# Kernel tuning notes

Measured on AMD Instinct MI355X. Metric: run time of the kernel, lower is better.

The kernel has to match this reference:

```python
import jax, jax.numpy as jnp
import numpy as np

N, CIN, COUT, E, NDIR = 65536, 128, 128, 589824, 9


def sel_conv(x, src, dst, sel, W, b):
    # x: [N, Cin]; W: [D, Cin, Cout]; edges j->i: out[i] += x[j] @ W[sel]
    n = x.shape[0]
    xs = x[src]  # [E, Cin] gather
    out = jnp.zeros((n, W.shape[2]), x.dtype)
    for d in range(W.shape[0]):  # fixed small direction count (9 or 1)
        m = (sel == d).astype(x.dtype)[:, None]
        agg = jax.ops.segment_sum(xs * m, dst, num_segments=n)  # [N, Cin]
        out = out + agg @ W[d]
    return out + b


def bn_eval(x, g, be, rm, rv, eps=1e-5):
    return (x - rm) * (g * jax.lax.rsqrt(rv + eps)) + be


def setup_inputs() -> dict:
    key = jax.random.key(0)
    ks = jax.random.split(key, 24)
    s = 0.05
    inp = {
        "x": jax.random.normal(ks[0], (N, CIN), jnp.float32),
        "edge_index": jax.random.randint(ks[1], (2, E), 0, N),
        "selections": jax.random.randint(ks[2], (E,), 0, NDIR),
        "W1": jax.random.normal(ks[3], (NDIR, CIN, COUT), jnp.float32) * s,
        "b1": jax.random.normal(ks[4], (COUT,), jnp.float32) * s,
        "g1": 1.0 + jax.random.normal(ks[5], (COUT,), jnp.float32) * s,
        "be1": jax.random.normal(ks[6], (COUT,), jnp.float32) * s,
        "rm1": jax.random.normal(ks[7], (COUT,), jnp.float32) * s,
        "rv1": 0.5 + jax.random.uniform(ks[8], (COUT,), jnp.float32),
        "W2": jax.random.normal(ks[9], (NDIR, COUT, COUT), jnp.float32) * s,
        "b2": jax.random.normal(ks[10], (COUT,), jnp.float32) * s,
        "g2": 1.0 + jax.random.normal(ks[11], (COUT,), jnp.float32) * s,
        "be2": jax.random.normal(ks[12], (COUT,), jnp.float32) * s,
        "rm2": jax.random.normal(ks[13], (COUT,), jnp.float32) * s,
        "rv2": 0.5 + jax.random.uniform(ks[14], (COUT,), jnp.float32),
        "W3": jax.random.normal(ks[15], (1, CIN, COUT), jnp.float32) * s,
        "b3": jax.random.normal(ks[16], (COUT,), jnp.float32) * s,
        "g3": 1.0 + jax.random.normal(ks[17], (COUT,), jnp.float32) * s,
        "be3": jax.random.normal(ks[18], (COUT,), jnp.float32) * s,
        "rm3": jax.random.normal(ks[19], (COUT,), jnp.float32) * s,
        "rv3": 0.5 + jax.random.uniform(ks[20], (COUT,), jnp.float32),
    }
    return inp


def reference(x, edge_index, selections, W1, b1, g1, be1, rm1, rv1,
              W2, b2, g2, be2, rm2, rv2, W3, b3, g3, be3, rm3, rv3):
    src, dst = edge_index[0], edge_index[1]
    # conv1: SelectionConv(3x3) + BN + ELU
    h = jax.nn.elu(bn_eval(sel_conv(x, src, dst, selections, W1, b1), g1, be1, rm1, rv1))
    # conv2: SelectionConv(3x3) + BN + ELU
    h = jax.nn.elu(bn_eval(sel_conv(h, src, dst, selections, W2, b2), g2, be2, rm2, rv2))
    # conv3: SelectionConv(1x1) shortcut (only selection-0 edges)
    sc = sel_conv(x, src, dst, selections, W3, b3)
    return jax.nn.elu(bn_eval(h + sc, g3, be3, rm3, rv3))
```

## Files before the change

### kernel.cpp

```cpp
#include <hip/hip_runtime.h>
#include <hip/hip_bf16.h>
#include <math.h>

#define N_NODES 65536
#define NDIR 9
#define NEDGE 589824
#define TILE_M 32
#define CAP 512
#define APITCH 136

typedef __attribute__((ext_vector_type(8))) short short8;
typedef __attribute__((ext_vector_type(4))) float f32x4;

__device__ inline float bf2f(unsigned short u){ return __uint_as_float(((unsigned int)u)<<16); }
__device__ inline unsigned short f2bf(float f){
  unsigned int x = __float_as_uint(f);
  x += 0x7fff + ((x>>16)&1);
  return (unsigned short)(x>>16);
}
__device__ inline float elu1(float x){ return x>0.f ? x : expm1f(x); }

__device__ inline void acc8(f32x4& a0, f32x4& a1, short8 v){
  a0[0] += bf2f((unsigned short)v[0]); a0[1] += bf2f((unsigned short)v[1]);
  a0[2] += bf2f((unsigned short)v[2]); a0[3] += bf2f((unsigned short)v[3]);
  a1[0] += bf2f((unsigned short)v[4]); a1[1] += bf2f((unsigned short)v[5]);
  a1[2] += bf2f((unsigned short)v[6]); a1[3] += bf2f((unsigned short)v[7]);
}

__global__ void prep_all(const float* __restrict__ x, unsigned short* __restrict__ xb,
                         const float* __restrict__ W1, const float* __restrict__ W2,
                         const float* __restrict__ W3,
                         const float* __restrict__ b1, const float* __restrict__ g1,
                         const float* __restrict__ be1, const float* __restrict__ rm1,
                         const float* __restrict__ rv1,
                         const float* __restrict__ b2, const float* __restrict__ g2,
                         const float* __restrict__ be2, const float* __restrict__ rm2,
                         const float* __restrict__ rv2,
                         const float* __restrict__ b3, const float* __restrict__ g3,
                         const float* __restrict__ be3, const float* __restrict__ rm3,
                         const float* __restrict__ rv3,
                         unsigned short* __restrict__ Wt1, unsigned short* __restrict__ Wt2,
                         float* __restrict__ bias1, float* __restrict__ bias2,
                         float* __restrict__ bias3, float* __restrict__ s3v,
                         int* __restrict__ hist){
  const float eps = 1e-5f;
  int b = blockIdx.x, tid = threadIdx.x;
  if (b < 64){
    int4 z = {0,0,0,0};
    *(int4*)&hist[(b*256 + tid)*4] = z;
  } else if (b < 1280){
    int idx = (b - 64)*256 + tid;
    if (idx < 1280*128) {
      int n = idx >> 7, k = idx & 127;
      float v;
      if (n < 1152) { int d = n >> 7, c = n & 127;
        float s = g1[c]*rsqrtf(rv1[c]+eps); v = W1[(d*128 + k)*128 + c] * s; }
      else { int c = n - 1152;
        float s = g3[c]*rsqrtf(rv3[c]+eps); v = W3[k*128 + c] * s; }
      Wt1[idx] = f2bf(v);
    } else {
      int j = idx - 1280*128;
      int n = j >> 7, k = j & 127;
      int d = n >> 7, c = n & 127;
      float s = g2[c]*rsqrtf(rv2[c]+eps);
      Wt2[j] = f2bf(W2[(d*128 + k)*128 + c] * s);
    }
  } else if (b == 1280){
    if (tid < 128){
      int c = tid;
      float s1 = g1[c]*rsqrtf(rv1[c]+eps);
      bias1[c] = (b1[c]-rm1[c])*s1 + be1[c];
      float s2 = g2[c]*rsqrtf(rv2[c]+eps);
      bias2[c] = (b2[c]-rm2[c])*s2 + be2[c];
      float s3 = g3[c]*rsqrtf(rv3[c]+eps);
      bias3[c] = (b3[c]-rm3[c])*s3 + be3[c];
      s3v[c] = s3;
    }
  } else {
    int i = ((b - 1281)*256 + tid)*8;
    f32x4 f0 = *(const f32x4*)(x + i);
    f32x4 f1 = *(const f32x4*)(x + i + 4);
    short8 t;
    #pragma unroll
    for (int j = 0; j < 4; j++){ t[j] = (short)f2bf(f0[j]); t[4+j] = (short)f2bf(f1[j]); }
    *(short8*)(xb + i) = t;
  }
}

__global__ void hist_k(const int* __restrict__ dst, int* __restrict__ hist){
  int e = blockIdx.x*256 + threadIdx.x;
  atomicAdd(&hist[dst[e]], 1);
}

__global__ void scan1_k(const int* __restrict__ in, int* __restrict__ out, int* __restrict__ bsum){
  __shared__ int wsum[4];
  int t = threadIdx.x;
  int base = blockIdx.x*1024 + t*4;
  int4 v = *(const int4*)(in + base);
  int s = v.x + v.y + v.z + v.w;
  int lane = t & 63, w = t >> 6;
  int inc = s;
  #pragma unroll
  for (int o = 1; o < 64; o <<= 1){ int n = __shfl_up(inc, o); if (lane >= o) inc += n; }
  if (lane == 63) wsum[w] = inc;
  __syncthreads();
  int acc = 0;
  for (int i = 0; i < w; i++) acc += wsum[i];
  int ex = acc + inc - s;
  out[base] = ex; out[base+1] = ex + v.x; out[base+2] = ex + v.x + v.y; out[base+3] = ex + v.x + v.y + v.z;
  if (t == 255) bsum[blockIdx.x] = acc + inc;
}

__global__ void scan3_k(int* __restrict__ rs, const int* __restrict__ bsumx, int* __restrict__ cursor){
  int i = blockIdx.x*256 + threadIdx.x;
  int v = rs[i] + bsumx[i >> 10];
  rs[i] = v; cursor[i] = v;
  if (i == 0) rs[N_NODES] = NEDGE;
}

__global__ void scatter_k(const int* __restrict__ src, const int* __restrict__ dst,
                          const int* __restrict__ sel,
                          int* __restrict__ cursor, int* __restrict__ sorted){
  int e = blockIdx.x*256 + threadIdx.x;
  int pos = atomicAdd(&cursor[dst[e]], 1);
  sorted[pos] = src[e] | (sel[e] << 16);
}

__device__ __forceinline__ void mfma_tile(f32x4 acc[2][2],
                                          const unsigned short* agg,
                                          const unsigned short* __restrict__ Wd,
                                          int w, int q, int r){
  #pragma unroll
  for (int kk = 0; kk < 4; kk++){
    const unsigned short* wp = Wd + (size_t)(w*32 + r)*128 + kk*32 + q*8;
    short8 b0 = *(const short8*)wp;
    short8 b1 = *(const short8*)(wp + 16*128);
    #pragma unroll
    for (int mt = 0; mt < 2; mt++){
      short8 av = *(const short8*)&agg[(mt*16 + r)*APITCH + kk*32 + q*8];
      acc[mt][0] = __builtin_amdgcn_mfma_f32_16x16x32_bf16(av, b0, acc[mt][0], 0, 0, 0);
      acc[mt][1] = __builtin_amdgcn_mfma_f32_16x16x32_bf16(av, b1, acc[mt][1], 0, 0, 0);
    }
  }
}

template<int IS_L2>
__global__ __launch_bounds__(256, 8) void layer_k(
    const unsigned short* __restrict__ H,
    const unsigned short* __restrict__ X,
    const unsigned short* __restrict__ Wf,
    const unsigned short* __restrict__ W3f,
    const int* __restrict__ rs, const int* __restrict__ sorted,
    const float* __restrict__ biasA, const float* __restrict__ bias3,
    const float* __restrict__ s3v,
    unsigned short* __restrict__ outB, float* __restrict__ outF){
  __shared__ __align__(16) unsigned short agg[TILE_M*APITCH];
  __shared__ int skey[CAP];
  __shared__ unsigned short skey2[CAP];
  __shared__ int rsl2[TILE_M + 1];
  __shared__ int po[TILE_M*9];
  __shared__ int wo[TILE_M*9];
  const int tid = threadIdx.x;
  const int w = tid >> 6, lane = tid & 63;
  const int q = lane >> 4, r = lane & 15;
  const int rid = tid >> 4, c = tid & 15;
  const int m0 = blockIdx.x * TILE_M;

  if (tid <= TILE_M) rsl2[tid] = rs[m0 + tid];
  for (int i = tid; i < TILE_M*9; i += 256) wo[i] = 0;
  __syncthreads();
  const int lo = rsl2[0];
  const int cnt = rsl2[TILE_M] - lo;
  for (int i = tid; i < cnt && i < CAP; i += 256) skey[i] = sorted[lo + i];
  __syncthreads();

  {
    const int nl8 = tid >> 3, sub = tid & 7;
    int s = rsl2[nl8] - lo, e = rsl2[nl8+1] - lo;
    if (e > CAP) e = CAP;
    for (int i = s + sub; i < e; i += 8)
      atomicAdd(&wo[nl8*9 + (skey[i] >> 16)], 1);
  }
  __syncthreads();
  if (tid < TILE_M){
    int base = rsl2[tid] - lo;
    if (base > CAP) base = CAP;
    #pragma unroll
    for (int d = 0; d < 9; d++){
      int b = tid*9 + d;
      po[b] = base;
      int cc = wo[b];
      wo[b] = base;
      base += cc;
    }
  }
  __syncthreads();
  {
    const int nl8 = tid >> 3, sub = tid & 7;
    int s = rsl2[nl8] - lo, e = rsl2[nl8+1] - lo;
    if (e > CAP) e = CAP;
    for (int i = s + sub; i < e; i += 8){
      int k = skey[i];
      int pos = atomicAdd(&wo[nl8*9 + (k >> 16)], 1);
      skey2[pos] = (unsigned short)k;
    }
  }
  __syncthreads();

  f32x4 acc[2][2];
  #pragma unroll
  for (int mt = 0; mt < 2; mt++){ acc[mt][0] = (f32x4){0,0,0,0}; acc[mt][1] = (f32x4){0,0,0,0}; }

  #pragma unroll 1
  for (int d = 0; d < 9; d++){
    if (d) __syncthreads();
    {
      int b = rid*9 + d;
      int s = po[b], e = wo[b];
      f32x4 a0 = {0,0,0,0}, a1 = {0,0,0,0};
      for (int i = s; i < e; i++){
        int key = skey2[i];
        short8 v = *(const short8*)(H + (size_t)key*128 + c*8);
        acc8(a0, a1, v);
      }
      int ts = rsl2[rid] - lo; if (ts < CAP) ts = CAP;
      int te = rsl2[rid+1] - lo;
      for (int i = ts; i < te; i++){
        int k = sorted[lo + i];
        if ((k >> 16) == d){
          short8 v = *(const short8*)(H + (size_t)(k & 0xFFFF)*128 + c*8);
          acc8(a0, a1, v);
        }
      }
      short8 o;
      o[0]=(short)f2bf(a0[0]); o[1]=(short)f2bf(a0[1]); o[2]=(short)f2bf(a0[2]); o[3]=(short)f2bf(a0[3]);
      o[4]=(short)f2bf(a1[0]); o[5]=(short)f2bf(a1[1]); o[6]=(short)f2bf(a1[2]); o[7]=(short)f2bf(a1[3]);
      *(short8*)&agg[rid*APITCH + c*8] = o;
    }
    {
      int b = (16 + rid)*9 + d;
      int s = po[b], e = wo[b];
      f32x4 a0 = {0,0,0,0}, a1 = {0,0,0,0};
      for (int i = s; i < e; i++){
        int key = skey2[i];
        short8 v = *(const short8*)(H + (size_t)key*128 + c*8);
        acc8(a0, a1, v);
      }
      int ts = rsl2[16+rid] - lo; if (ts < CAP) ts = CAP;
      int te = rsl2[16+rid+1] - lo;
      for (int i = ts; i < te; i++){
        int k = sorted[lo + i];
        if ((k >> 16) == d){
          short8 v = *(const short8*)(H + (size_t)(k & 0xFFFF)*128 + c*8);
          acc8(a0, a1, v);
        }
      }
      short8 o;
      o[0]=(short)f2bf(a0[0]); o[1]=(short)f2bf(a0[1]); o[2]=(short)f2bf(a0[2]); o[3]=(short)f2bf(a0[3]);
      o[4]=(short)f2bf(a1[0]); o[5]=(short)f2bf(a1[1]); o[6]=(short)f2bf(a1[2]); o[7]=(short)f2bf(a1[3]);
      *(short8*)&agg[(16 + rid)*APITCH + c*8] = o;
    }
    __syncthreads();
    mfma_tile(acc, agg, Wf + (size_t)d*128*128, w, q, r);
  }

  if constexpr (!IS_L2){
    #pragma unroll
    for (int mt = 0; mt < 2; mt++)
      #pragma unroll
      for (int n2 = 0; n2 < 2; n2++){
        int col = w*32 + n2*16 + r;
        float bA = biasA[col];
        #pragma unroll
        for (int rr = 0; rr < 4; rr++){
          int row = m0 + mt*16 + q*4 + rr;
          outB[(size_t)row*128 + col] = f2bf(elu1(acc[mt][n2][rr] + bA));
        }
      }
  } else {
    __syncthreads();
    #pragma unroll
    for (int t2 = 0; t2 < 2; t2++){
      int nl = t2*16 + rid;
      int b = nl*9;
      int s = po[b], e = wo[b];
      f32x4 a0 = {0,0,0,0}, a1 = {0,0,0,0};
      for (int i = s; i < e; i++){
        int key = skey2[i];
        short8 v = *(const short8*)(X + (size_t)key*128 + c*8);
        acc8(a0, a1, v);
      }
      int ts = rsl2[nl] - lo; if (ts < CAP) ts = CAP;
      int te = rsl2[nl+1] - lo;
      for (int i = ts; i < te; i++){
        int k = sorted[lo + i];
        if ((k >> 16) == 0){
          short8 v = *(const short8*)(X + (size_t)(k & 0xFFFF)*128 + c*8);
          acc8(a0, a1, v);
        }
      }
      short8 o;
      o[0]=(short)f2bf(a0[0]); o[1]=(short)f2bf(a0[1]); o[2]=(short)f2bf(a0[2]); o[3]=(short)f2bf(a0[3]);
      o[4]=(short)f2bf(a1[0]); o[5]=(short)f2bf(a1[1]); o[6]=(short)f2bf(a1[2]); o[7]=(short)f2bf(a1[3]);
      *(short8*)&agg[nl*APITCH + c*8] = o;
    }
    __syncthreads();
    f32x4 sca[2][2];
    #pragma unroll
    for (int mt = 0; mt < 2; mt++){ sca[mt][0] = (f32x4){0,0,0,0}; sca[mt][1] = (f32x4){0,0,0,0}; }
    mfma_tile(sca, agg, W3f, w, q, r);
    #pragma unroll
    for (int mt = 0; mt < 2; mt++)
      #pragma unroll
      for (int n2 = 0; n2 < 2; n2++){
        int col = w*32 + n2*16 + r;
        float bA = biasA[col], b3 = bias3[col], s3 = s3v[col];
        #pragma unroll
        for (int rr = 0; rr < 4; rr++){
          int row = m0 + mt*16 + q*4 + rr;
          float h = elu1(acc[mt][n2][rr] + bA);
          outF[(size_t)row*128 + col] = elu1(h*s3 + sca[mt][n2][rr] + b3);
        }
      }
  }
}

extern "C" void kernel_launch(void* const* d_in, const int* in_sizes, int n_in,
                              void* d_out, int out_size, void* d_ws, size_t ws_size,
                              hipStream_t stream){
  const float* x   = (const float*)d_in[0];
  const int*   ei  = (const int*)d_in[1];
  const int*   sel = (const int*)d_in[2];
  const float* W1  = (const float*)d_in[3];
  const float* b1  = (const float*)d_in[4];
  const float* g1  = (const float*)d_in[5];
  const float* be1 = (const float*)d_in[6];
  const float* rm1 = (const float*)d_in[7];
  const float* rv1 = (const float*)d_in[8];
  const float* W2  = (const float*)d_in[9];
  const float* b2  = (const float*)d_in[10];
  const float* g2  = (const float*)d_in[11];
  const float* be2 = (const float*)d_in[12];
  const float* rm2 = (const float*)d_in[13];
  const float* rv2 = (const float*)d_in[14];
  const float* W3  = (const float*)d_in[15];
  const float* b3  = (const float*)d_in[16];
  const float* g3  = (const float*)d_in[17];
  const float* be3 = (const float*)d_in[18];
  const float* rm3 = (const float*)d_in[19];
  const float* rv3 = (const float*)d_in[20];

  char* ws = (char*)d_ws;
  unsigned short* xb   = (unsigned short*)(ws);
  unsigned short* h1   = (unsigned short*)(ws + 16777216);
  unsigned short* Wt1  = (unsigned short*)(ws + 33554432);
  unsigned short* Wt2  = (unsigned short*)(ws + 33882112);
  float* bias1  = (float*)(ws + 34177024);
  float* bias2  = bias1 + 128;
  float* bias3  = bias1 + 256;
  float* s3v    = bias1 + 384;
  int* hist     = (int*)(ws + 34179072);
  int* rs       = (int*)(ws + 36538368);
  int* cursor   = (int*)(ws + 38897920);
  int* bsum     = (int*)(ws + 41257216);
  int* bsumx    = (int*)(ws + 41261312);
  int* bsumT    = (int*)(ws + 41265408);
  int* sorted   = (int*)(ws + 41265664);

  const int* srcp = ei;
  const int* dstp = ei + NEDGE;

  prep_all<<<5377, 256, 0, stream>>>(x, xb, W1, W2, W3,
                                     b1, g1, be1, rm1, rv1,
                                     b2, g2, be2, rm2, rv2,
                                     b3, g3, be3, rm3, rv3,
                                     Wt1, Wt2, bias1, bias2, bias3, s3v, hist);
  hist_k<<<NEDGE/256, 256, 0, stream>>>(dstp, hist);
  scan1_k<<<N_NODES/1024, 256, 0, stream>>>(hist, rs, bsum);
  scan1_k<<<1, 256, 0, stream>>>(bsum, bsumx, bsumT);
  scan3_k<<<N_NODES/256, 256, 0, stream>>>(rs, bsumx, cursor);
  scatter_k<<<NEDGE/256, 256, 0, stream>>>(srcp, dstp, sel, cursor, sorted);

  layer_k<0><<<2048, 256, 0, stream>>>(xb, nullptr, Wt1, nullptr, rs, sorted,
                                       bias1, nullptr, nullptr, h1, nullptr);
  layer_k<1><<<2048, 256, 0, stream>>>(h1, xb, Wt2, Wt1 + 1152*128, rs, sorted,
                                       bias2, bias3, s3v, nullptr, (float*)d_out);
}
```

Before: 364.0 us.

## Fuse preprocessing, histogram, scan and scatter into one cooperative kernel

Replaces six separate launches (prep, histogram, two scan passes, scan fixup, scatter) with a single cooperative kernel of 1024 blocks that uses grid-stride loops and grid.sync() between phases. This removes per-launch overhead and the gaps between small kernels. In exchange, the grid-wide barriers cost time, occupancy is limited to a co-resident grid, and the single-block scan phases leave most blocks idle.

```diff
diff --git a/kernel.cpp b/kernel.cpp
--- a/kernel.cpp
+++ b/kernel.cpp
@@ -1,6 +1,9 @@
 #include <hip/hip_runtime.h>
 #include <hip/hip_bf16.h>
+#include <hip/hip_cooperative_groups.h>
 #include <math.h>
+
+namespace cg = cooperative_groups;
 
 #define N_NODES 65536
 #define NDIR 9
@@ -27,29 +30,38 @@
   a1[2] += bf2f((unsigned short)v[6]); a1[3] += bf2f((unsigned short)v[7]);
 }
 
-__global__ void prep_all(const float* __restrict__ x, unsigned short* __restrict__ xb,
-                         const float* __restrict__ W1, const float* __restrict__ W2,
-                         const float* __restrict__ W3,
-                         const float* __restrict__ b1, const float* __restrict__ g1,
-                         const float* __restrict__ be1, const float* __restrict__ rm1,
-                         const float* __restrict__ rv1,
-                         const float* __restrict__ b2, const float* __restrict__ g2,
-                         const float* __restrict__ be2, const float* __restrict__ rm2,
-                         const float* __restrict__ rv2,
-                         const float* __restrict__ b3, const float* __restrict__ g3,
-                         const float* __restrict__ be3, const float* __restrict__ rm3,
-                         const float* __restrict__ rv3,
-                         unsigned short* __restrict__ Wt1, unsigned short* __restrict__ Wt2,
-                         float* __restrict__ bias1, float* __restrict__ bias2,
-                         float* __restrict__ bias3, float* __restrict__ s3v,
-                         int* __restrict__ hist){
+__global__ __launch_bounds__(256, 4) void chain_k(
+    const float* __restrict__ x, unsigned short* __restrict__ xb,
+    const float* __restrict__ W1, const float* __restrict__ W2,
+    const float* __restrict__ W3,
+    const float* __restrict__ b1, const float* __restrict__ g1,
+    const float* __restrict__ be1, const float* __restrict__ rm1,
+    const float* __restrict__ rv1,
+    const float* __restrict__ b2, const float* __restrict__ g2,
+    const float* __restrict__ be2, const float* __restrict__ rm2,
+    const float* __restrict__ rv2,
+    const float* __restrict__ b3, const float* __restrict__ g3,
+    const float* __restrict__ be3, const float* __restrict__ rm3,
+    const float* __restrict__ rv3,
+    unsigned short* __restrict__ Wt1, unsigned short* __restrict__ Wt2,
+    float* __restrict__ bias1, float* __restrict__ bias2,
+    float* __restrict__ bias3, float* __restrict__ s3v,
+    int* __restrict__ hist, int* __restrict__ rs, int* __restrict__ cursor,
+    int* __restrict__ bsum, int* __restrict__ bsumx,
+    const int* __restrict__ src, const int* __restrict__ dst,
+    const int* __restrict__ sel, int* __restrict__ sorted){
+  cg::grid_group grid = cg::this_grid();
+  __shared__ int wsum[4];
   const float eps = 1e-5f;
-  int b = blockIdx.x, tid = threadIdx.x;
-  if (b < 64){
+  const int b = blockIdx.x, tid = threadIdx.x;
+  const int gtid = b*256 + tid;
+  const int gstride = gridDim.x*256;
+
+  for (int i = gtid; i < N_NODES/4; i += gstride){
     int4 z = {0,0,0,0};
-    *(int4*)&hist[(b*256 + tid)*4] = z;
-  } else if (b < 1280){
-    int idx = (b - 64)*256 + tid;
+    ((int4*)hist)[i] = z;
+  }
+  for (int idx = gtid; idx < (1280*128 + 1152*128); idx += gstride){
     if (idx < 1280*128) {
       int n = idx >> 7, k = idx & 127;
       float v;
@@ -65,65 +77,69 @@
       float s = g2[c]*rsqrtf(rv2[c]+eps);
       Wt2[j] = f2bf(W2[(d*128 + k)*128 + c] * s);
     }
-  } else if (b == 1280){
-    if (tid < 128){
-      int c = tid;
-      float s1 = g1[c]*rsqrtf(rv1[c]+eps);
-      bias1[c] = (b1[c]-rm1[c])*s1 + be1[c];
-      float s2 = g2[c]*rsqrtf(rv2[c]+eps);
-      bias2[c] = (b2[c]-rm2[c])*s2 + be2[c];
-      float s3 = g3[c]*rsqrtf(rv3[c]+eps);
-      bias3[c] = (b3[c]-rm3[c])*s3 + be3[c];
-      s3v[c] = s3;
-    }
-  } else {
-    int i = ((b - 1281)*256 + tid)*8;
-    f32x4 f0 = *(const f32x4*)(x + i);
-    f32x4 f1 = *(const f32x4*)(x + i + 4);
+  }
+  if (gtid < 128){
+    int c = gtid;
+    float s1 = g1[c]*rsqrtf(rv1[c]+eps);
+    bias1[c] = (b1[c]-rm1[c])*s1 + be1[c];
+    float s2 = g2[c]*rsqrtf(rv2[c]+eps);
+    bias2[c] = (b2[c]-rm2[c])*s2 + be2[c];
+    float s3 = g3[c]*rsqrtf(rv3[c]+eps);
+    bias3[c] = (b3[c]-rm3[c])*s3 + be3[c];
+    s3v[c] = s3;
+  }
+  for (int i = gtid; i < N_NODES*128/8; i += gstride){
+    f32x4 f0 = *(const f32x4*)(x + i*8);
+    f32x4 f1 = *(const f32x4*)(x + i*8 + 4);
     short8 t;
     #pragma unroll
     for (int j = 0; j < 4; j++){ t[j] = (short)f2bf(f0[j]); t[4+j] = (short)f2bf(f1[j]); }
-    *(short8*)(xb + i) = t;
-  }
-}
-
-__global__ void hist_k(const int* __restrict__ dst, int* __restrict__ hist){
-  int e = blockIdx.x*256 + threadIdx.x;
-  atomicAdd(&hist[dst[e]], 1);
-}
-
-__global__ void scan1_k(const int* __restrict__ in, int* __restrict__ out, int* __restrict__ bsum){
-  __shared__ int wsum[4];
-  int t = threadIdx.x;
-  int base = blockIdx.x*1024 + t*4;
-  int4 v = *(const int4*)(in + base);
-  int s = v.x + v.y + v.z + v.w;
-  int lane = t & 63, w = t >> 6;
-  int inc = s;
-  #pragma unroll
-  for (int o = 1; o < 64; o <<= 1){ int n = __shfl_up(inc, o); if (lane >= o) inc += n; }
-  if (lane == 63) wsum[w] = inc;
-  __syncthreads();
-  int acc = 0;
-  for (int i = 0; i < w; i++) acc += wsum[i];
-  int ex = acc + inc - s;
-  out[base] = ex; out[base+1] = ex + v.x; out[base+2] = ex + v.x + v.y; out[base+3] = ex + v.x + v.y + v.z;
-  if (t == 255) bsum[blockIdx.x] = acc + inc;
-}
-
-__global__ void scan3_k(int* __restrict__ rs, const int* __restrict__ bsumx, int* __restrict__ cursor){
-  int i = blockIdx.x*256 + threadIdx.x;
-  int v = rs[i] + bsumx[i >> 10];
-  rs[i] = v; cursor[i] = v;
-  if (i == 0) rs[N_NODES] = NEDGE;
-}
-
-__global__ void scatter_k(const int* __restrict__ src, const int* __restrict__ dst,
-                          const int* __restrict__ sel,
-                          int* __restrict__ cursor, int* __restrict__ sorted){
-  int e = blockIdx.x*256 + threadIdx.x;
-  int pos = atomicAdd(&cursor[dst[e]], 1);
-  sorted[pos] = src[e] | (sel[e] << 16);
+    *(short8*)(xb + i*8) = t;
+  }
+  grid.sync();
+
+  for (int e = gtid; e < NEDGE; e += gstride)
+    atomicAdd(&hist[dst[e]], 1);
+  grid.sync();
+
+  if (b < 64){
+    int base = b*1024 + tid*4;
+    int4 v = *(const int4*)(hist + base);
+    int s = v.x + v.y + v.z + v.w;
+    int lane = tid & 63, w = tid >> 6;
+    int inc = s;
+    #pragma unroll
+    for (int o = 1; o < 64; o <<= 1){ int n = __shfl_up(inc, o); if (lane >= o) inc += n; }
+    if (lane == 63) wsum[w] = inc;
+    __syncthreads();
+    int acc = 0;
+    for (int i = 0; i < w; i++) acc += wsum[i];
+    int ex = acc + inc - s;
+    rs[base] = ex; rs[base+1] = ex + v.x; rs[base+2] = ex + v.x + v.y; rs[base+3] = ex + v.x + v.y + v.z;
+    if (tid == 255) bsum[b] = acc + inc;
+  }
+  grid.sync();
+
+  if (b == 0 && tid < 64){
+    int v = bsum[tid];
+    int inc = v;
+    #pragma unroll
+    for (int o = 1; o < 64; o <<= 1){ int n = __shfl_up(inc, o); if (tid >= o) inc += n; }
+    bsumx[tid] = inc - v;
+  }
+  grid.sync();
+
+  for (int i = gtid; i < N_NODES; i += gstride){
+    int v = rs[i] + bsumx[i >> 10];
+    rs[i] = v; cursor[i] = v;
+  }
+  if (gtid == 0) rs[N_NODES] = NEDGE;
+  grid.sync();
+
+  for (int e = gtid; e < NEDGE; e += gstride){
+    int pos = atomicAdd(&cursor[dst[e]], 1);
+    sorted[pos] = src[e] | (sel[e] << 16);
+  }
 }
 
 __device__ __forceinline__ void mfma_tile(f32x4 acc[2][2],
@@ -364,22 +380,23 @@
   int* cursor   = (int*)(ws + 38897920);
   int* bsum     = (int*)(ws + 41257216);
   int* bsumx    = (int*)(ws + 41261312);
-  int* bsumT    = (int*)(ws + 41265408);
   int* sorted   = (int*)(ws + 41265664);
 
   const int* srcp = ei;
   const int* dstp = ei + NEDGE;
 
-  prep_all<<<5377, 256, 0, stream>>>(x, xb, W1, W2, W3,
-                                     b1, g1, be1, rm1, rv1,
-                                     b2, g2, be2, rm2, rv2,
-                                     b3, g3, be3, rm3, rv3,
-                                     Wt1, Wt2, bias1, bias2, bias3, s3v, hist);
-  hist_k<<<NEDGE/256, 256, 0, stream>>>(dstp, hist);
-  scan1_k<<<N_NODES/1024, 256, 0, stream>>>(hist, rs, bsum);
-  scan1_k<<<1, 256, 0, stream>>>(bsum, bsumx, bsumT);
-  scan3_k<<<N_NODES/256, 256, 0, stream>>>(rs, bsumx, cursor);
-  scatter_k<<<NEDGE/256, 256, 0, stream>>>(srcp, dstp, sel, cursor, sorted);
+  void* args[] = {
+    (void*)&x, (void*)&xb, (void*)&W1, (void*)&W2, (void*)&W3,
+    (void*)&b1, (void*)&g1, (void*)&be1, (void*)&rm1, (void*)&rv1,
+    (void*)&b2, (void*)&g2, (void*)&be2, (void*)&rm2, (void*)&rv2,
+    (void*)&b3, (void*)&g3, (void*)&be3, (void*)&rm3, (void*)&rv3,
+    (void*)&Wt1, (void*)&Wt2, (void*)&bias1, (void*)&bias2,
+    (void*)&bias3, (void*)&s3v,
+    (void*)&hist, (void*)&rs, (void*)&cursor, (void*)&bsum, (void*)&bsumx,
+    (void*)&srcp, (void*)&dstp, (void*)&sel, (void*)&sorted
+  };
+  hipLaunchCooperativeKernel((const void*)chain_k, dim3(1024), dim3(256),
+                             args, 0, stream);
 
   layer_k<0><<<2048, 256, 0, stream>>>(xb, nullptr, Wt1, nullptr, rs, sorted,
                                        bias1, nullptr, nullptr, h1, nullptr);
```

Result: slower. 905.6 us (+148.8%).

## Replace CSR build with fixed-slot per-node edge buckets plus overflow list

Applied to the files above, without the earlier changes.

Drops the histogram, two-level prefix scan and cursor kernels. Edges are now scattered straight into fixed 24-slot per-node buckets via an atomic counter, and any extra edges go to a global overflow list. The layer kernels read bucket counts and slots directly, and every thread scans the whole overflow list for matching (node, direction) entries. This removes several launches and passes over the edge data. In exchange the bucket array is padded, and cost grows with overflow size. Correctness also relies on the overflow staying under its fixed cap.

```diff
diff --git a/kernel.cpp b/kernel.cpp
--- a/kernel.cpp
+++ b/kernel.cpp
@@ -6,7 +6,8 @@
 #define NDIR 9
 #define NEDGE 589824
 #define TILE_M 32
-#define CAP 512
+#define SLOTS 24
+#define OCAP 65536
 #define APITCH 136
 
 typedef __attribute__((ext_vector_type(8))) short short8;
@@ -42,12 +43,12 @@
                          unsigned short* __restrict__ Wt1, unsigned short* __restrict__ Wt2,
                          float* __restrict__ bias1, float* __restrict__ bias2,
                          float* __restrict__ bias3, float* __restrict__ s3v,
-                         int* __restrict__ hist){
+                         int* __restrict__ cnt, int* __restrict__ ocnt){
   const float eps = 1e-5f;
   int b = blockIdx.x, tid = threadIdx.x;
   if (b < 64){
     int4 z = {0,0,0,0};
-    *(int4*)&hist[(b*256 + tid)*4] = z;
+    *(int4*)&cnt[(b*256 + tid)*4] = z;
   } else if (b < 1280){
     int idx = (b - 64)*256 + tid;
     if (idx < 1280*128) {
@@ -75,6 +76,8 @@
       float s3 = g3[c]*rsqrtf(rv3[c]+eps);
       bias3[c] = (b3[c]-rm3[c])*s3 + be3[c];
       s3v[c] = s3;
+    } else if (tid == 128){
+      *ocnt = 0;
     }
   } else {
     int i = ((b - 1281)*256 + tid)*8;
@@ -87,43 +90,20 @@
   }
 }
 
-__global__ void hist_k(const int* __restrict__ dst, int* __restrict__ hist){
-  int e = blockIdx.x*256 + threadIdx.x;
-  atomicAdd(&hist[dst[e]], 1);
-}
-
-__global__ void scan1_k(const int* __restrict__ in, int* __restrict__ out, int* __restrict__ bsum){
-  __shared__ int wsum[4];
-  int t = threadIdx.x;
-  int base = blockIdx.x*1024 + t*4;
-  int4 v = *(const int4*)(in + base);
-  int s = v.x + v.y + v.z + v.w;
-  int lane = t & 63, w = t >> 6;
-  int inc = s;
-  #pragma unroll
-  for (int o = 1; o < 64; o <<= 1){ int n = __shfl_up(inc, o); if (lane >= o) inc += n; }
-  if (lane == 63) wsum[w] = inc;
-  __syncthreads();
-  int acc = 0;
-  for (int i = 0; i < w; i++) acc += wsum[i];
-  int ex = acc + inc - s;
-  out[base] = ex; out[base+1] = ex + v.x; out[base+2] = ex + v.x + v.y; out[base+3] = ex + v.x + v.y + v.z;
-  if (t == 255) bsum[blockIdx.x] = acc + inc;
-}
-
-__global__ void scan3_k(int* __restrict__ rs, const int* __restrict__ bsumx, int* __restrict__ cursor){
-  int i = blockIdx.x*256 + threadIdx.x;
-  int v = rs[i] + bsumx[i >> 10];
-  rs[i] = v; cursor[i] = v;
-  if (i == 0) rs[N_NODES] = NEDGE;
-}
-
 __global__ void scatter_k(const int* __restrict__ src, const int* __restrict__ dst,
                           const int* __restrict__ sel,
-                          int* __restrict__ cursor, int* __restrict__ sorted){
+                          int* __restrict__ cnt, int* __restrict__ sorted,
+                          int* __restrict__ ocnt, int* __restrict__ overflow){
   int e = blockIdx.x*256 + threadIdx.x;
-  int pos = atomicAdd(&cursor[dst[e]], 1);
-  sorted[pos] = src[e] | (sel[e] << 16);
+  int d = dst[e];
+  int key = src[e] | (sel[e] << 16);
+  int pos = atomicAdd(&cnt[d], 1);
+  if (pos < SLOTS){
+    sorted[d*SLOTS + pos] = key;
+  } else {
+    int oi = atomicAdd(ocnt, 1);
+    if (oi < OCAP){ overflow[oi*2] = d; overflow[oi*2 + 1] = key; }
+  }
 }
 
 __device__ __forceinline__ void mfma_tile(f32x4 acc[2][2],
@@ -150,41 +130,41 @@
     const unsigned short* __restrict__ X,
     const unsigned short* __restrict__ Wf,
     const unsigned short* __restrict__ W3f,
-    const int* __restrict__ rs, const int* __restrict__ sorted,
+    const int* __restrict__ cntg, const int* __restrict__ sorted,
+    const int* __restrict__ ocnt, const int* __restrict__ overflow,
     const float* __restrict__ biasA, const float* __restrict__ bias3,
     const float* __restrict__ s3v,
     unsigned short* __restrict__ outB, float* __restrict__ outF){
   __shared__ __align__(16) unsigned short agg[TILE_M*APITCH];
-  __shared__ int skey[CAP];
-  __shared__ unsigned short skey2[CAP];
-  __shared__ int rsl2[TILE_M + 1];
+  __shared__ int skey[TILE_M*SLOTS];
+  __shared__ unsigned short skey2[TILE_M*SLOTS];
+  __shared__ int cnts[TILE_M];
   __shared__ int po[TILE_M*9];
   __shared__ int wo[TILE_M*9];
+  __shared__ int ocs;
   const int tid = threadIdx.x;
   const int w = tid >> 6, lane = tid & 63;
   const int q = lane >> 4, r = lane & 15;
   const int rid = tid >> 4, c = tid & 15;
   const int m0 = blockIdx.x * TILE_M;
 
-  if (tid <= TILE_M) rsl2[tid] = rs[m0 + tid];
+  if (tid < TILE_M){ int v = cntg[m0 + tid]; cnts[tid] = v < SLOTS ? v : SLOTS; }
+  if (tid == 255){ int v = *ocnt; ocs = v < OCAP ? v : OCAP; }
   for (int i = tid; i < TILE_M*9; i += 256) wo[i] = 0;
   __syncthreads();
-  const int lo = rsl2[0];
-  const int cnt = rsl2[TILE_M] - lo;
-  for (int i = tid; i < cnt && i < CAP; i += 256) skey[i] = sorted[lo + i];
-  __syncthreads();
 
   {
     const int nl8 = tid >> 3, sub = tid & 7;
-    int s = rsl2[nl8] - lo, e = rsl2[nl8+1] - lo;
-    if (e > CAP) e = CAP;
-    for (int i = s + sub; i < e; i += 8)
-      atomicAdd(&wo[nl8*9 + (skey[i] >> 16)], 1);
+    int e8 = cnts[nl8];
+    for (int j = sub; j < e8; j += 8){
+      int k = sorted[(m0 + nl8)*SLOTS + j];
+      skey[nl8*SLOTS + j] = k;
+      atomicAdd(&wo[nl8*9 + (k >> 16)], 1);
+    }
   }
   __syncthreads();
   if (tid < TILE_M){
-    int base = rsl2[tid] - lo;
-    if (base > CAP) base = CAP;
+    int base = tid*SLOTS;
     #pragma unroll
     for (int d = 0; d < 9; d++){
       int b = tid*9 + d;
@@ -197,10 +177,9 @@
   __syncthreads();
   {
     const int nl8 = tid >> 3, sub = tid & 7;
-    int s = rsl2[nl8] - lo, e = rsl2[nl8+1] - lo;
-    if (e > CAP) e = CAP;
-    for (int i = s + sub; i < e; i += 8){
-      int k = skey[i];
+    int e8 = cnts[nl8];
+    for (int j = sub; j < e8; j += 8){
+      int k = skey[nl8*SLOTS + j];
       int pos = atomicAdd(&wo[nl8*9 + (k >> 16)], 1);
       skey2[pos] = (unsigned short)k;
     }
@@ -223,12 +202,9 @@
         short8 v = *(const short8*)(H + (size_t)key*128 + c*8);
         acc8(a0, a1, v);
       }
-      int ts = rsl2[rid] - lo; if (ts < CAP) ts = CAP;
-      int te = rsl2[rid+1] - lo;
-      for (int i = ts; i < te; i++){
-        int k = sorted[lo + i];
-        if ((k >> 16) == d){
-          short8 v = *(const short8*)(H + (size_t)(k & 0xFFFF)*128 + c*8);
+      for (int i = 0; i < ocs; i++){
+        if (overflow[i*2] == m0 + rid && (overflow[i*2+1] >> 16) == d){
+          short8 v = *(const short8*)(H + (size_t)(overflow[i*2+1] & 0xFFFF)*128 + c*8);
           acc8(a0, a1, v);
         }
       }
@@ -246,12 +222,9 @@
         short8 v = *(const short8*)(H + (size_t)key*128 + c*8);
         acc8(a0, a1, v);
       }
-      int ts = rsl2[16+rid] - lo; if (ts < CAP) ts = CAP;
-      int te = rsl2[16+rid+1] - lo;
-      for (int i = ts; i < te; i++){
-        int k = sorted[lo + i];
-        if ((k >> 16) == d){
-          short8 v = *(const short8*)(H + (size_t)(k & 0xFFFF)*128 + c*8);
+      for (int i = 0; i < ocs; i++){
+        if (overflow[i*2] == m0 + 16 + rid && (overflow[i*2+1] >> 16) == d){
+          short8 v = *(const short8*)(H + (size_t)(overflow[i*2+1] & 0xFFFF)*128 + c*8);
           acc8(a0, a1, v);
         }
       }
@@ -290,12 +263,9 @@
         short8 v = *(const short8*)(X + (size_t)key*128 + c*8);
         acc8(a0, a1, v);
       }
-      int ts = rsl2[nl] - lo; if (ts < CAP) ts = CAP;
-      int te = rsl2[nl+1] - lo;
-      for (int i = ts; i < te; i++){
-        int k = sorted[lo + i];
-        if ((k >> 16) == 0){
-          short8 v = *(const short8*)(X + (size_t)(k & 0xFFFF)*128 + c*8);
+      for (int i = 0; i < ocs; i++){
+        if (overflow[i*2] == m0 + nl && (overflow[i*2+1] >> 16) == 0){
+          short8 v = *(const short8*)(X + (size_t)(overflow[i*2+1] & 0xFFFF)*128 + c*8);
           acc8(a0, a1, v);
         }
       }
@@ -359,13 +329,10 @@
   float* bias2  = bias1 + 128;
   float* bias3  = bias1 + 256;
   float* s3v    = bias1 + 384;
-  int* hist     = (int*)(ws + 34179072);
-  int* rs       = (int*)(ws + 36538368);
-  int* cursor   = (int*)(ws + 38897920);
-  int* bsum     = (int*)(ws + 41257216);
-  int* bsumx    = (int*)(ws + 41261312);
-  int* bsumT    = (int*)(ws + 41265408);
-  int* sorted   = (int*)(ws + 41265664);
+  int* cnt      = (int*)(ws + 34179072);
+  int* ocnt     = (int*)(ws + 34441216);
+  int* overflow = (int*)(ws + 34441472);
+  int* sorted   = (int*)(ws + 34965760);
 
   const int* srcp = ei;
   const int* dstp = ei + NEDGE;
@@ -374,15 +341,14 @@
                                      b1, g1, be1, rm1, rv1,
                                      b2, g2, be2, rm2, rv2,
                                      b3, g3, be3, rm3, rv3,
-                                     Wt1, Wt2, bias1, bias2, bias3, s3v, hist);
-  hist_k<<<NEDGE/256, 256, 0, stream>>>(dstp, hist);
-  scan1_k<<<N_NODES/1024, 256, 0, stream>>>(hist, rs, bsum);
-  scan1_k<<<1, 256, 0, stream>>>(bsum, bsumx, bsumT);
-  scan3_k<<<N_NODES/256, 256, 0, stream>>>(rs, bsumx, cursor);
-  scatter_k<<<NEDGE/256, 256, 0, stream>>>(srcp, dstp, sel, cursor, sorted);
-
-  layer_k<0><<<2048, 256, 0, stream>>>(xb, nullptr, Wt1, nullptr, rs, sorted,
+                                     Wt1, Wt2, bias1, bias2, bias3, s3v,
+                                     cnt, ocnt);
+  scatter_k<<<NEDGE/256, 256, 0, stream>>>(srcp, dstp, sel, cnt, sorted, ocnt, overflow);
+
+  layer_k<0><<<2048, 256, 0, stream>>>(xb, nullptr, Wt1, nullptr, cnt, sorted,
+                                       ocnt, overflow,
                                        bias1, nullptr, nullptr, h1, nullptr);
-  layer_k<1><<<2048, 256, 0, stream>>>(h1, xb, Wt2, Wt1 + 1152*128, rs, sorted,
+  layer_k<1><<<2048, 256, 0, stream>>>(h1, xb, Wt2, Wt1 + 1152*128, cnt, sorted,
+                                       ocnt, overflow,
                                        bias2, bias3, s3v, nullptr, (float*)d_out);
 }
```

Measured after the change: 332.5 us. 8.7% less time.
